# Kernel optimization log

Hardware: AMD Instinct MI355X
Metric: run time of the kernel (lower is better)

The kernel has to match this reference:

```python
import jax, jax.numpy as jnp
import numpy as np

ENCODER_DIM, DECODER_DIM, ATTN_DIM = 2048, 512, 512
B, P = 128, 196  # batch, num_pixels (14x14)


def setup_inputs() -> dict:
    key = jax.random.key(0)
    ks = jax.random.split(key, 8)
    s_e = 1.0 / np.sqrt(ENCODER_DIM)
    s_d = 1.0 / np.sqrt(DECODER_DIM)
    s_a = 1.0 / np.sqrt(ATTN_DIM)
    return {
        "encoder_out": jax.random.normal(ks[0], (B, P, ENCODER_DIM), jnp.float32),
        "decoder_hidden": jax.random.normal(ks[1], (B, DECODER_DIM), jnp.float32),
        "W_enc": jax.random.uniform(ks[2], (ENCODER_DIM, ATTN_DIM), jnp.float32, -s_e, s_e),
        "b_enc": jax.random.uniform(ks[3], (ATTN_DIM,), jnp.float32, -s_e, s_e),
        "W_dec": jax.random.uniform(ks[4], (DECODER_DIM, ATTN_DIM), jnp.float32, -s_d, s_d),
        "b_dec": jax.random.uniform(ks[5], (ATTN_DIM,), jnp.float32, -s_d, s_d),
        "W_full": jax.random.uniform(ks[6], (ATTN_DIM,), jnp.float32, -s_a, s_a),
        "b_full": jax.random.uniform(ks[7], (), jnp.float32, -s_a, s_a),
    }


def reference(encoder_out, decoder_hidden, W_enc, b_enc, W_dec, b_dec, W_full, b_full):
    # att1: [B, P, A]; att2: [B, A]
    att1 = jnp.einsum("bpe,ea->bpa", encoder_out, W_enc) + b_enc
    att2 = decoder_hidden @ W_dec + b_dec
    # broadcast add + relu + score projection -> [B, P]
    att = jax.nn.relu(att1 + att2[:, None, :]) @ W_full + b_full
    alpha = jax.nn.softmax(att, axis=1)  # over pixels
    # weighted sum over pixels -> [B, E]
    attention_weighted_encoding = jnp.einsum("bpe,bp->be", encoder_out, alpha)
    return (attention_weighted_encoding, alpha)
```

## Files before the change

### kernel.cpp

```cpp
#include <hip/hip_runtime.h>
#include <hip/hip_bf16.h>

#define ENC_DIM 2048
#define DEC_DIM 512
#define ATT_DIM 512
#define BATCH   128
#define NPIX    196
#define NROWS   (BATCH * NPIX)

typedef short bf16x8 __attribute__((ext_vector_type(8)));
typedef float f32x4  __attribute__((ext_vector_type(4)));
typedef unsigned short u16x8 __attribute__((ext_vector_type(8)));

__device__ __forceinline__ unsigned short f2bf(float f) {
    union { float f; unsigned u; } v; v.f = f;
    unsigned r = v.u + 0x7fffu + ((v.u >> 16) & 1u);
    return (unsigned short)(r >> 16);
}

__global__ void k0_transpose(const float* __restrict__ W_enc,
                             unsigned short* __restrict__ Wt) {
    __shared__ float ts[64][65];
    const int a0 = blockIdx.x * 64;
    const int e0 = blockIdx.y * 64;
    const int tx = threadIdx.x & 15;
    const int ty = threadIdx.x >> 4;
    #pragma unroll
    for (int p = 0; p < 4; ++p) {
        const int e = ty + p * 16;
        const float4 v = *(const float4*)&W_enc[(size_t)(e0 + e) * ATT_DIM + a0 + tx * 4];
        ts[e][tx * 4 + 0] = v.x; ts[e][tx * 4 + 1] = v.y;
        ts[e][tx * 4 + 2] = v.z; ts[e][tx * 4 + 3] = v.w;
    }
    __syncthreads();
    #pragma unroll
    for (int p = 0; p < 4; ++p) {
        const int a = ty + p * 16;
        ushort4 u;
        u.x = f2bf(ts[tx * 4 + 0][a]);
        u.y = f2bf(ts[tx * 4 + 1][a]);
        u.z = f2bf(ts[tx * 4 + 2][a]);
        u.w = f2bf(ts[tx * 4 + 3][a]);
        *(ushort4*)&Wt[(size_t)(a0 + a) * ENC_DIM + e0 + tx * 4] = u;
    }
}

__global__ void k1_att2(const float* __restrict__ dh, const float* __restrict__ W_dec,
                        const float* __restrict__ b_dec, const float* __restrict__ b_enc,
                        const float* __restrict__ b_full,
                        float* __restrict__ att2, float* __restrict__ att) {
    __shared__ float dhs[DEC_DIM];
    const int b = blockIdx.x, t = threadIdx.x;
    dhs[t]       = dh[b * DEC_DIM + t];
    dhs[t + 256] = dh[b * DEC_DIM + t + 256];
    __syncthreads();
    float acc0 = 0.f, acc1 = 0.f;
    for (int d = 0; d < DEC_DIM; ++d) {
        const float h = dhs[d];
        acc0 += h * W_dec[d * ATT_DIM + t];
        acc1 += h * W_dec[d * ATT_DIM + t + 256];
    }
    att2[b * ATT_DIM + t]       = acc0 + b_dec[t]       + b_enc[t];
    att2[b * ATT_DIM + t + 256] = acc1 + b_dec[t + 256] + b_enc[t + 256];
    const int gid = b * 256 + t;
    if (gid < NROWS) att[gid] = b_full[0];
}

__launch_bounds__(256, 4)
__global__ void k2_gemm(const float* __restrict__ enc, const unsigned short* __restrict__ Wt,
                        const float* __restrict__ att2, const float* __restrict__ W_full,
                        float* __restrict__ att) {
    __shared__ __align__(16) unsigned short As[64 * 72];
    __shared__ __align__(16) unsigned short Bs[128 * 72];
    __shared__ float att2s[2][128];
    __shared__ float wfs[128];

    const int t    = threadIdx.x;
    const int n0   = blockIdx.x * 128;
    const int row0 = blockIdx.y * 64;
    const int b0   = row0 / NPIX;
    const int rows_left = (b0 + 1) * NPIX - row0;

    if (t < 128) {
        att2s[0][t] = att2[b0 * ATT_DIM + n0 + t];
        att2s[1][t] = (b0 + 1 < BATCH) ? att2[(b0 + 1) * ATT_DIM + n0 + t] : 0.f;
        wfs[t]      = W_full[n0 + t];
    }

    const int w    = t >> 6;
    const int lane = t & 63;
    const int q    = lane >> 4;
    const int cl   = lane & 15;
    const int wm   = (w >> 1) * 32;
    const int wn   = (w & 1) * 64;

    f32x4 acc[2][4] = {};

    const int ar = t >> 3;
    const int ak = (t & 7) * 8;
    const int bn = t >> 2;
    const int bk = (t & 3) * 16;

    const float*          encA = enc + (size_t)(row0 + ar) * ENC_DIM + ak;
    const unsigned short* WtB  = Wt  + (size_t)(n0 + bn)   * ENC_DIM + bk;

    for (int k0 = 0; k0 < ENC_DIM; k0 += 64) {
        __syncthreads();
        #pragma unroll
        for (int p = 0; p < 2; ++p) {
            const float4 v0 = *(const float4*)(encA + (size_t)p * 32 * ENC_DIM + k0);
            const float4 v1 = *(const float4*)(encA + (size_t)p * 32 * ENC_DIM + k0 + 4);
            u16x8 u;
            u[0] = f2bf(v0.x); u[1] = f2bf(v0.y); u[2] = f2bf(v0.z); u[3] = f2bf(v0.w);
            u[4] = f2bf(v1.x); u[5] = f2bf(v1.y); u[6] = f2bf(v1.z); u[7] = f2bf(v1.w);
            *(u16x8*)&As[(ar + p * 32) * 72 + ak] = u;
        }
        #pragma unroll
        for (int p = 0; p < 2; ++p) {
            const uint4 v0 = *(const uint4*)(WtB + (size_t)p * 64 * ENC_DIM + k0);
            const uint4 v1 = *(const uint4*)(WtB + (size_t)p * 64 * ENC_DIM + k0 + 8);
            *(uint4*)&Bs[(bn + p * 64) * 72 + bk]     = v0;
            *(uint4*)&Bs[(bn + p * 64) * 72 + bk + 8] = v1;
        }
        __syncthreads();

        #pragma unroll
        for (int h = 0; h < 2; ++h) {
            bf16x8 af[2], bfr[4];
            #pragma unroll
            for (int i = 0; i < 2; ++i)
                af[i]  = *(const bf16x8*)&As[(wm + i * 16 + cl) * 72 + h * 32 + q * 8];
            #pragma unroll
            for (int i = 0; i < 4; ++i)
                bfr[i] = *(const bf16x8*)&Bs[(wn + i * 16 + cl) * 72 + h * 32 + q * 8];
            #pragma unroll
            for (int mi = 0; mi < 2; ++mi)
                #pragma unroll
                for (int ni = 0; ni < 4; ++ni)
                    acc[mi][ni] = __builtin_amdgcn_mfma_f32_16x16x32_bf16(
                        af[mi], bfr[ni], acc[mi][ni], 0, 0, 0);
        }
    }

    #pragma unroll
    for (int mi = 0; mi < 2; ++mi) {
        float rs[4];
        #pragma unroll
        for (int i = 0; i < 4; ++i) {
            const int lr  = wm + mi * 16 + q * 4 + i;
            const int sel = (lr >= rows_left) ? 1 : 0;
            float sum = 0.f;
            #pragma unroll
            for (int ni = 0; ni < 4; ++ni) {
                const int j = wn + ni * 16 + cl;
                float v = acc[mi][ni][i] + att2s[sel][j];
                v = fmaxf(v, 0.f);
                sum += v * wfs[j];
            }
            rs[i] = sum;
        }
        #pragma unroll
        for (int o = 1; o < 16; o <<= 1) {
            #pragma unroll
            for (int i = 0; i < 4; ++i) rs[i] += __shfl_xor(rs[i], o);
        }
        if (cl == 0) {
            #pragma unroll
            for (int i = 0; i < 4; ++i) {
                const int r = row0 + wm + mi * 16 + q * 4 + i;
                atomicAdd(&att[r], rs[i]);
            }
        }
    }
}

__global__ void k3_softmax(float* __restrict__ att_alpha) {
    __shared__ float red[4];
    const int b = blockIdx.x, t = threadIdx.x;
    const int w = t >> 6, lane = t & 63;
    const float x = (t < NPIX) ? att_alpha[b * NPIX + t] : -INFINITY;
    float m = x;
    #pragma unroll
    for (int o = 32; o >= 1; o >>= 1) m = fmaxf(m, __shfl_xor(m, o));
    if (lane == 0) red[w] = m;
    __syncthreads();
    m = fmaxf(fmaxf(red[0], red[1]), fmaxf(red[2], red[3]));
    const float e = (t < NPIX) ? __expf(x - m) : 0.f;
    float s = e;
    #pragma unroll
    for (int o = 32; o >= 1; o >>= 1) s += __shfl_xor(s, o);
    __syncthreads();
    if (lane == 0) red[w] = s;
    __syncthreads();
    s = red[0] + red[1] + red[2] + red[3];
    if (t < NPIX) att_alpha[b * NPIX + t] = e / s;
}

__global__ void k4_awe(const float* __restrict__ enc, const float* __restrict__ alpha,
                       float* __restrict__ awe) {
    __shared__ float as[NPIX];
    const int b  = blockIdx.y;
    const int t  = threadIdx.x;
    const int e0 = blockIdx.x * 512 + t * 4;
    as[t] = alpha[b * NPIX + t];
    if (t < NPIX - 128) as[t + 128] = alpha[b * NPIX + t + 128];
    __syncthreads();
    const float* base = enc + (size_t)b * NPIX * ENC_DIM + e0;
    f32x4 a[8] = {};
    for (int p = 0; p < 192; p += 8) {
        #pragma unroll
        for (int j = 0; j < 8; ++j) {
            const f32x4 v = *(const f32x4*)(base + (size_t)(p + j) * ENC_DIM);
            a[j] += as[p + j] * v;
        }
    }
    #pragma unroll
    for (int j = 0; j < 4; ++j) {
        const f32x4 v = *(const f32x4*)(base + (size_t)(192 + j) * ENC_DIM);
        a[j] += as[192 + j] * v;
    }
    const f32x4 r = ((a[0] + a[1]) + (a[2] + a[3])) + ((a[4] + a[5]) + (a[6] + a[7]));
    *(f32x4*)&awe[(size_t)b * ENC_DIM + e0] = r;
}

extern "C" void kernel_launch(void* const* d_in, const int* in_sizes, int n_in,
                              void* d_out, int out_size, void* d_ws, size_t ws_size,
                              hipStream_t stream) {
    const float* enc    = (const float*)d_in[0];
    const float* dh     = (const float*)d_in[1];
    const float* W_enc  = (const float*)d_in[2];
    const float* b_enc  = (const float*)d_in[3];
    const float* W_dec  = (const float*)d_in[4];
    const float* b_dec  = (const float*)d_in[5];
    const float* W_full = (const float*)d_in[6];
    const float* b_full = (const float*)d_in[7];

    float* awe   = (float*)d_out;
    float* alpha = awe + BATCH * ENC_DIM;

    unsigned short* Wt   = (unsigned short*)d_ws;
    float*          att2 = (float*)((char*)d_ws + (size_t)ATT_DIM * ENC_DIM * 2);

    k0_transpose<<<dim3(8, 32),  256, 0, stream>>>(W_enc, Wt);
    k1_att2     <<<128,          256, 0, stream>>>(dh, W_dec, b_dec, b_enc, b_full, att2, alpha);
    k2_gemm     <<<dim3(4, 392), 256, 0, stream>>>(enc, Wt, att2, W_full, alpha);
    k3_softmax  <<<128,          256, 0, stream>>>(alpha);
    k4_awe      <<<dim3(4, 128), 128, 0, stream>>>(enc, alpha, awe);
}
```

Measured before the change: 435.5 us.

## Restructure GEMM to full-N row tiles with pre-fragmented weights and double buffering

The GEMM kernel now has each 512-thread block own 128 rows and all 512 attention columns. Previously four blocks each re-read and re-converted the same fp32 encoder rows. The weights are pre-packed into the MFMA fragment order, so each wave loads its B fragments straight into registers without LDS. The A tile is double-buffered in LDS with register prefetch. The att2 and awe kernels are also re-split for more parallelism, and the bf16 conversion now uses a library intrinsic. The risks are lower occupancy from 128 accumulator registers per thread and a grid of only 196 blocks.

```diff
diff --git a/kernel.cpp b/kernel.cpp
--- a/kernel.cpp
+++ b/kernel.cpp
@@ -18,31 +18,33 @@
     return (unsigned short)(r >> 16);
 }
 
-__global__ void k0_transpose(const float* __restrict__ W_enc,
-                             unsigned short* __restrict__ Wt) {
-    __shared__ float ts[64][65];
-    const int a0 = blockIdx.x * 64;
-    const int e0 = blockIdx.y * 64;
-    const int tx = threadIdx.x & 15;
-    const int ty = threadIdx.x >> 4;
-    #pragma unroll
-    for (int p = 0; p < 4; ++p) {
-        const int e = ty + p * 16;
-        const float4 v = *(const float4*)&W_enc[(size_t)(e0 + e) * ATT_DIM + a0 + tx * 4];
-        ts[e][tx * 4 + 0] = v.x; ts[e][tx * 4 + 1] = v.y;
-        ts[e][tx * 4 + 2] = v.z; ts[e][tx * 4 + 3] = v.w;
-    }
-    __syncthreads();
-    #pragma unroll
-    for (int p = 0; p < 4; ++p) {
-        const int a = ty + p * 16;
-        ushort4 u;
-        u.x = f2bf(ts[tx * 4 + 0][a]);
-        u.y = f2bf(ts[tx * 4 + 1][a]);
-        u.z = f2bf(ts[tx * 4 + 2][a]);
-        u.w = f2bf(ts[tx * 4 + 3][a]);
-        *(ushort4*)&Wt[(size_t)(a0 + a) * ENC_DIM + e0 + tx * 4] = u;
-    }
+__device__ __forceinline__ unsigned short bfc(float f) {
+    union { __hip_bfloat16 h; unsigned short u; } v;
+    v.h = __float2bfloat16(f);
+    return v.u;
+}
+
+__global__ void k0_wtfrag(const float* __restrict__ W_enc,
+                          unsigned short* __restrict__ Wtf) {
+    const int slot = blockIdx.x * 256 + threadIdx.x;
+    const int lane = slot & 63;
+    const int cg   = (slot >> 6) & 31;
+    const int h    = (slot >> 11) & 1;
+    const int s    = slot >> 12;
+    const int q = lane >> 4, cl = lane & 15;
+    const int a = cg * 16 + cl;
+    const int k = s * 64 + h * 32 + q * 8;
+    ushort4 u0, u1;
+    u0.x = f2bf(W_enc[(size_t)(k + 0) * ATT_DIM + a]);
+    u0.y = f2bf(W_enc[(size_t)(k + 1) * ATT_DIM + a]);
+    u0.z = f2bf(W_enc[(size_t)(k + 2) * ATT_DIM + a]);
+    u0.w = f2bf(W_enc[(size_t)(k + 3) * ATT_DIM + a]);
+    u1.x = f2bf(W_enc[(size_t)(k + 4) * ATT_DIM + a]);
+    u1.y = f2bf(W_enc[(size_t)(k + 5) * ATT_DIM + a]);
+    u1.z = f2bf(W_enc[(size_t)(k + 6) * ATT_DIM + a]);
+    u1.w = f2bf(W_enc[(size_t)(k + 7) * ATT_DIM + a]);
+    *(ushort4*)&Wtf[(size_t)slot * 8]     = u0;
+    *(ushort4*)&Wtf[(size_t)slot * 8 + 4] = u1;
 }
 
 __global__ void k1_att2(const float* __restrict__ dh, const float* __restrict__ W_dec,
@@ -50,112 +52,133 @@
                         const float* __restrict__ b_full,
                         float* __restrict__ att2, float* __restrict__ att) {
     __shared__ float dhs[DEC_DIM];
-    const int b = blockIdx.x, t = threadIdx.x;
+    const int bid = blockIdx.x, t = threadIdx.x;
+    const int b = bid >> 1;
+    const int c = (bid & 1) * 256 + t;
     dhs[t]       = dh[b * DEC_DIM + t];
     dhs[t + 256] = dh[b * DEC_DIM + t + 256];
     __syncthreads();
     float acc0 = 0.f, acc1 = 0.f;
-    for (int d = 0; d < DEC_DIM; ++d) {
-        const float h = dhs[d];
-        acc0 += h * W_dec[d * ATT_DIM + t];
-        acc1 += h * W_dec[d * ATT_DIM + t + 256];
-    }
-    att2[b * ATT_DIM + t]       = acc0 + b_dec[t]       + b_enc[t];
-    att2[b * ATT_DIM + t + 256] = acc1 + b_dec[t + 256] + b_enc[t + 256];
-    const int gid = b * 256 + t;
+    #pragma unroll 8
+    for (int d = 0; d < 256; ++d) {
+        acc0 += dhs[d]       * W_dec[d * ATT_DIM + c];
+        acc1 += dhs[d + 256] * W_dec[(d + 256) * ATT_DIM + c];
+    }
+    att2[b * ATT_DIM + c] = acc0 + acc1 + b_dec[c] + b_enc[c];
+    const int gid = bid * 256 + t;
     if (gid < NROWS) att[gid] = b_full[0];
 }
 
-__launch_bounds__(256, 4)
-__global__ void k2_gemm(const float* __restrict__ enc, const unsigned short* __restrict__ Wt,
+__launch_bounds__(512, 2)
+__global__ void k2_gemm(const float* __restrict__ enc, const unsigned short* __restrict__ Wtf,
                         const float* __restrict__ att2, const float* __restrict__ W_full,
                         float* __restrict__ att) {
-    __shared__ __align__(16) unsigned short As[64 * 72];
-    __shared__ __align__(16) unsigned short Bs[128 * 72];
-    __shared__ float att2s[2][128];
-    __shared__ float wfs[128];
+    __shared__ __align__(16) unsigned short As0[128 * 72];
+    __shared__ __align__(16) unsigned short As1[128 * 72];
+    __shared__ float att2s[2][ATT_DIM];
+    __shared__ float wfs[ATT_DIM];
 
     const int t    = threadIdx.x;
-    const int n0   = blockIdx.x * 128;
-    const int row0 = blockIdx.y * 64;
+    const int row0 = blockIdx.x * 128;
     const int b0   = row0 / NPIX;
     const int rows_left = (b0 + 1) * NPIX - row0;
 
-    if (t < 128) {
-        att2s[0][t] = att2[b0 * ATT_DIM + n0 + t];
-        att2s[1][t] = (b0 + 1 < BATCH) ? att2[(b0 + 1) * ATT_DIM + n0 + t] : 0.f;
-        wfs[t]      = W_full[n0 + t];
-    }
+    att2s[0][t] = att2[b0 * ATT_DIM + t];
+    att2s[1][t] = (b0 + 1 < BATCH) ? att2[(b0 + 1) * ATT_DIM + t] : 0.f;
+    wfs[t]      = W_full[t];
 
     const int w    = t >> 6;
     const int lane = t & 63;
     const int q    = lane >> 4;
     const int cl   = lane & 15;
-    const int wm   = (w >> 1) * 32;
-    const int wn   = (w & 1) * 64;
-
-    f32x4 acc[2][4] = {};
-
-    const int ar = t >> 3;
-    const int ak = (t & 7) * 8;
-    const int bn = t >> 2;
-    const int bk = (t & 3) * 16;
-
-    const float*          encA = enc + (size_t)(row0 + ar) * ENC_DIM + ak;
-    const unsigned short* WtB  = Wt  + (size_t)(n0 + bn)   * ENC_DIM + bk;
-
-    for (int k0 = 0; k0 < ENC_DIM; k0 += 64) {
-        __syncthreads();
+
+    const int arow = t >> 2;
+    const int acq  = (t & 3) * 16;
+    const float* encA = enc + (size_t)(row0 + arow) * ENC_DIM + acq;
+
+    f32x4 acc[8][4] = {};
+    bf16x8 bA[2][4], bB[2][4];
+
+    {
+        const float4 v0 = *(const float4*)(encA + 0);
+        const float4 v1 = *(const float4*)(encA + 4);
+        const float4 v2 = *(const float4*)(encA + 8);
+        const float4 v3 = *(const float4*)(encA + 12);
+        u16x8 u0, u1;
+        u0[0]=bfc(v0.x); u0[1]=bfc(v0.y); u0[2]=bfc(v0.z); u0[3]=bfc(v0.w);
+        u0[4]=bfc(v1.x); u0[5]=bfc(v1.y); u0[6]=bfc(v1.z); u0[7]=bfc(v1.w);
+        u1[0]=bfc(v2.x); u1[1]=bfc(v2.y); u1[2]=bfc(v2.z); u1[3]=bfc(v2.w);
+        u1[4]=bfc(v3.x); u1[5]=bfc(v3.y); u1[6]=bfc(v3.z); u1[7]=bfc(v3.w);
+        *(u16x8*)&As0[arow * 72 + acq]     = u0;
+        *(u16x8*)&As0[arow * 72 + acq + 8] = u1;
         #pragma unroll
-        for (int p = 0; p < 2; ++p) {
-            const float4 v0 = *(const float4*)(encA + (size_t)p * 32 * ENC_DIM + k0);
-            const float4 v1 = *(const float4*)(encA + (size_t)p * 32 * ENC_DIM + k0 + 4);
-            u16x8 u;
-            u[0] = f2bf(v0.x); u[1] = f2bf(v0.y); u[2] = f2bf(v0.z); u[3] = f2bf(v0.w);
-            u[4] = f2bf(v1.x); u[5] = f2bf(v1.y); u[6] = f2bf(v1.z); u[7] = f2bf(v1.w);
-            *(u16x8*)&As[(ar + p * 32) * 72 + ak] = u;
-        }
-        #pragma unroll
-        for (int p = 0; p < 2; ++p) {
-            const uint4 v0 = *(const uint4*)(WtB + (size_t)p * 64 * ENC_DIM + k0);
-            const uint4 v1 = *(const uint4*)(WtB + (size_t)p * 64 * ENC_DIM + k0 + 8);
-            *(uint4*)&Bs[(bn + p * 64) * 72 + bk]     = v0;
-            *(uint4*)&Bs[(bn + p * 64) * 72 + bk + 8] = v1;
-        }
-        __syncthreads();
-
-        #pragma unroll
-        for (int h = 0; h < 2; ++h) {
-            bf16x8 af[2], bfr[4];
-            #pragma unroll
-            for (int i = 0; i < 2; ++i)
-                af[i]  = *(const bf16x8*)&As[(wm + i * 16 + cl) * 72 + h * 32 + q * 8];
-            #pragma unroll
-            for (int i = 0; i < 4; ++i)
-                bfr[i] = *(const bf16x8*)&Bs[(wn + i * 16 + cl) * 72 + h * 32 + q * 8];
-            #pragma unroll
-            for (int mi = 0; mi < 2; ++mi)
-                #pragma unroll
-                for (int ni = 0; ni < 4; ++ni)
-                    acc[mi][ni] = __builtin_amdgcn_mfma_f32_16x16x32_bf16(
-                        af[mi], bfr[ni], acc[mi][ni], 0, 0, 0);
-        }
-    }
+        for (int h = 0; h < 2; ++h)
+            #pragma unroll
+            for (int ni = 0; ni < 4; ++ni)
+                bA[h][ni] = *(const bf16x8*)&Wtf[(size_t)h * 16384
+                                                 + (w * 4 + ni) * 512 + lane * 8];
+    }
+    __syncthreads();
+
+#define K2_BODY(CURAS, NXTAS, CURB, NXTB, KK, PF)                                   \
+    {                                                                               \
+        float4 aL0, aL1, aL2, aL3;                                                  \
+        if (PF) {                                                                   \
+            const float* ap = encA + (KK) + 64;                                     \
+            aL0 = *(const float4*)(ap + 0);  aL1 = *(const float4*)(ap + 4);        \
+            aL2 = *(const float4*)(ap + 8);  aL3 = *(const float4*)(ap + 12);       \
+            const size_t bo = (size_t)((KK) + 64) * 512;                            \
+            _Pragma("unroll")                                                       \
+            for (int h = 0; h < 2; ++h)                                             \
+                _Pragma("unroll")                                                   \
+                for (int ni = 0; ni < 4; ++ni)                                      \
+                    NXTB[h][ni] = *(const bf16x8*)&Wtf[bo + (size_t)h * 16384       \
+                                                       + (w * 4 + ni) * 512         \
+                                                       + lane * 8];                 \
+        }                                                                           \
+        _Pragma("unroll")                                                           \
+        for (int h = 0; h < 2; ++h)                                                 \
+            _Pragma("unroll")                                                       \
+            for (int mi = 0; mi < 8; ++mi) {                                        \
+                const bf16x8 af = *(const bf16x8*)&CURAS[(mi * 16 + cl) * 72        \
+                                                         + h * 32 + q * 8];         \
+                _Pragma("unroll")                                                   \
+                for (int ni = 0; ni < 4; ++ni)                                      \
+                    acc[mi][ni] = __builtin_amdgcn_mfma_f32_16x16x32_bf16(          \
+                        af, CURB[h][ni], acc[mi][ni], 0, 0, 0);                     \
+            }                                                                       \
+        if (PF) {                                                                   \
+            u16x8 u0, u1;                                                           \
+            u0[0]=bfc(aL0.x); u0[1]=bfc(aL0.y); u0[2]=bfc(aL0.z); u0[3]=bfc(aL0.w); \
+            u0[4]=bfc(aL1.x); u0[5]=bfc(aL1.y); u0[6]=bfc(aL1.z); u0[7]=bfc(aL1.w); \
+            u1[0]=bfc(aL2.x); u1[1]=bfc(aL2.y); u1[2]=bfc(aL2.z); u1[3]=bfc(aL2.w); \
+            u1[4]=bfc(aL3.x); u1[5]=bfc(aL3.y); u1[6]=bfc(aL3.z); u1[7]=bfc(aL3.w); \
+            *(u16x8*)&NXTAS[arow * 72 + acq]     = u0;                              \
+            *(u16x8*)&NXTAS[arow * 72 + acq + 8] = u1;                              \
+        }                                                                           \
+        __syncthreads();                                                            \
+    }
+
+    for (int kk = 0; kk < ENC_DIM; kk += 128) {
+        K2_BODY(As0, As1, bA, bB, kk, true);
+        K2_BODY(As1, As0, bB, bA, kk + 64, (kk + 128 < ENC_DIM));
+    }
+#undef K2_BODY
 
     #pragma unroll
-    for (int mi = 0; mi < 2; ++mi) {
+    for (int mi = 0; mi < 8; ++mi) {
         float rs[4];
         #pragma unroll
         for (int i = 0; i < 4; ++i) {
-            const int lr  = wm + mi * 16 + q * 4 + i;
+            const int lr  = mi * 16 + q * 4 + i;
             const int sel = (lr >= rows_left) ? 1 : 0;
             float sum = 0.f;
             #pragma unroll
             for (int ni = 0; ni < 4; ++ni) {
-                const int j = wn + ni * 16 + cl;
-                float v = acc[mi][ni][i] + att2s[sel][j];
+                const int c = w * 64 + ni * 16 + cl;
+                float v = acc[mi][ni][i] + att2s[sel][c];
                 v = fmaxf(v, 0.f);
-                sum += v * wfs[j];
+                sum += v * wfs[c];
             }
             rs[i] = sum;
         }
@@ -167,7 +190,7 @@
         if (cl == 0) {
             #pragma unroll
             for (int i = 0; i < 4; ++i) {
-                const int r = row0 + wm + mi * 16 + q * 4 + i;
+                const int r = row0 + mi * 16 + q * 4 + i;
                 atomicAdd(&att[r], rs[i]);
             }
         }
@@ -199,28 +222,31 @@
 __global__ void k4_awe(const float* __restrict__ enc, const float* __restrict__ alpha,
                        float* __restrict__ awe) {
     __shared__ float as[NPIX];
+    __shared__ f32x4 red[4][64];
     const int b  = blockIdx.y;
     const int t  = threadIdx.x;
-    const int e0 = blockIdx.x * 512 + t * 4;
-    as[t] = alpha[b * NPIX + t];
-    if (t < NPIX - 128) as[t + 128] = alpha[b * NPIX + t + 128];
+    const int s  = t & 63;
+    const int g  = t >> 6;
+    const int e0 = blockIdx.x * 256 + s * 4;
+    if (t < NPIX) as[t] = alpha[b * NPIX + t];
     __syncthreads();
     const float* base = enc + (size_t)b * NPIX * ENC_DIM + e0;
-    f32x4 a[8] = {};
-    for (int p = 0; p < 192; p += 8) {
-        #pragma unroll
-        for (int j = 0; j < 8; ++j) {
-            const f32x4 v = *(const f32x4*)(base + (size_t)(p + j) * ENC_DIM);
-            a[j] += as[p + j] * v;
-        }
-    }
-    #pragma unroll
-    for (int j = 0; j < 4; ++j) {
-        const f32x4 v = *(const f32x4*)(base + (size_t)(192 + j) * ENC_DIM);
-        a[j] += as[192 + j] * v;
-    }
-    const f32x4 r = ((a[0] + a[1]) + (a[2] + a[3])) + ((a[4] + a[5]) + (a[6] + a[7]));
-    *(f32x4*)&awe[(size_t)b * ENC_DIM + e0] = r;
+    f32x4 a0 = {}, a1 = {}, a2 = {}, a3 = {};
+    int p = g;
+    #pragma unroll 4
+    for (int it = 0; it < 12; ++it, p += 16) {
+        a0 += as[p]      * *(const f32x4*)(base + (size_t)(p)      * ENC_DIM);
+        a1 += as[p + 4]  * *(const f32x4*)(base + (size_t)(p + 4)  * ENC_DIM);
+        a2 += as[p + 8]  * *(const f32x4*)(base + (size_t)(p + 8)  * ENC_DIM);
+        a3 += as[p + 12] * *(const f32x4*)(base + (size_t)(p + 12) * ENC_DIM);
+    }
+    a0 += as[p] * *(const f32x4*)(base + (size_t)p * ENC_DIM);
+    red[g][s] = (a0 + a1) + (a2 + a3);
+    __syncthreads();
+    if (g == 0) {
+        const f32x4 r = (red[0][s] + red[1][s]) + (red[2][s] + red[3][s]);
+        *(f32x4*)&awe[(size_t)b * ENC_DIM + e0] = r;
+    }
 }
 
 extern "C" void kernel_launch(void* const* d_in, const int* in_sizes, int n_in,
@@ -238,12 +264,12 @@
     float* awe   = (float*)d_out;
     float* alpha = awe + BATCH * ENC_DIM;
 
-    unsigned short* Wt   = (unsigned short*)d_ws;
+    unsigned short* Wtf  = (unsigned short*)d_ws;
     float*          att2 = (float*)((char*)d_ws + (size_t)ATT_DIM * ENC_DIM * 2);
 
-    k0_transpose<<<dim3(8, 32),  256, 0, stream>>>(W_enc, Wt);
-    k1_att2     <<<128,          256, 0, stream>>>(dh, W_dec, b_dec, b_enc, b_full, att2, alpha);
-    k2_gemm     <<<dim3(4, 392), 256, 0, stream>>>(enc, Wt, att2, W_full, alpha);
+    k0_wtfrag   <<<512,          256, 0, stream>>>(W_enc, Wtf);
+    k1_att2     <<<256,          256, 0, stream>>>(dh, W_dec, b_dec, b_enc, b_full, att2, alpha);
+    k2_gemm     <<<196,          512, 0, stream>>>(enc, Wtf, att2, W_full, alpha);
     k3_softmax  <<<128,          256, 0, stream>>>(alpha);
-    k4_awe      <<<dim3(4, 128), 128, 0, stream>>>(enc, alpha, awe);
-}
+    k4_awe      <<<dim3(8, 128), 256, 0, stream>>>(enc, alpha, awe);
+}
```

New measurement: 531.7 us. 1.22x slower.
